# Kernel tuning notes

Hardware: AMD Instinct MI355X
Metric: run time of the kernel (lower is better)

The kernel has to match this reference:

```python
import jax, jax.numpy as jnp
import numpy as np

N, D, NUM_CLASSES = 4096, 512, 128
MARGIN = 0.3


def setup_inputs() -> dict:
    key = jax.random.key(0)
    k1, k2 = jax.random.split(key)
    embeddings = jax.random.normal(k1, (N, D), dtype=jnp.float32)
    labels = jax.random.randint(k2, (N,), 0, NUM_CLASSES, dtype=jnp.int64)
    return {"embeddings": embeddings, "labels": labels}


def _batch_hard_triplet(embeddings, labels, margin):
    # L2-normalize rows (torch F.normalize: x / max(||x||, eps))
    norm = jnp.linalg.norm(embeddings, axis=1, keepdims=True)
    e = embeddings / jnp.maximum(norm, 1e-12)
    n = e.shape[0]
    # Pairwise Euclidean distance via Gram matrix; ||a-b||^2 = 2 - 2 a.b for unit vectors
    gram = e @ e.T                                   # [N, N]
    sq = jnp.clip(2.0 - 2.0 * gram, 0.0, None)
    # safe sqrt: zero (and exactly-equal) pairs get distance 0 with zero gradient
    nz = sq > 0
    dist = jnp.where(nz, jnp.sqrt(jnp.where(nz, sq, 1.0)), 0.0)  # [N, N]

    same = labels[:, None] == labels[None, :]        # [N, N] bool
    eye = jnp.eye(n, dtype=bool)
    pos_mask = same & ~eye                           # positives excluding self
    neg_mask = ~same

    # hardest positive (row max over positives), hardest negative (row min over negatives)
    dist_ap = jnp.max(jnp.where(pos_mask, dist, -jnp.inf), axis=1)  # [N]
    dist_an = jnp.min(jnp.where(neg_mask, dist, jnp.inf), axis=1)   # [N]

    valid = jnp.any(pos_mask, axis=1) & jnp.any(neg_mask, axis=1)   # rows kept by torch loop
    per_row = jax.nn.relu(dist_ap - dist_an + margin)
    num_valid = jnp.sum(valid)
    loss_sum = jnp.sum(jnp.where(valid, per_row, 0.0))
    return jnp.where(num_valid > 0, loss_sum / jnp.maximum(num_valid, 1), 0.0)


def reference(embeddings, labels):
    return _batch_hard_triplet(embeddings, labels, MARGIN)
```

## Files before the change

### kernel.cpp

```cpp
#include <hip/hip_runtime.h>
#include <hip/hip_bf16.h>
#include <stdint.h>


#define NROW 4096
#define DIM  512
#define MARGIN 0.3f
#define BT 128
#define BK 32
#define NTILE (NROW / BT)
#define NPAIR (NTILE * (NTILE + 1) / 2)
#define POS_INIT 0xFFFFFFFFu
#define NEG_INIT 0u

typedef __attribute__((ext_vector_type(8))) __bf16 bf16x8;
typedef __attribute__((ext_vector_type(4))) float  f32x4;

__device__ __forceinline__ unsigned enc(float f) {
    unsigned u = __float_as_uint(f);
    return (u & 0x80000000u) ? ~u : (u | 0x80000000u);
}
__device__ __forceinline__ float dec(unsigned e) {
    return (e & 0x80000000u) ? __uint_as_float(e & 0x7fffffffu)
                             : __uint_as_float(~e);
}

__device__ __forceinline__ unsigned short f2bf(float f) {
    __hip_bfloat16 h = __float2bfloat16(f);
    return *reinterpret_cast<unsigned short*>(&h);
}

__device__ __forceinline__ void async_copy16(const void* g, void* l) {
    __builtin_amdgcn_global_load_lds(
        (const __attribute__((address_space(1))) unsigned int*)g,
        (__attribute__((address_space(3))) unsigned int*)l,
        16, 0, 0);
}

__global__ void tl_norm(const float* __restrict__ E,
                        __hip_bfloat16* __restrict__ Ebf,
                        unsigned* __restrict__ posArr,
                        unsigned* __restrict__ negArr) {
    if (blockIdx.x < 16) {
        int t = blockIdx.x * 256 + threadIdx.x;
        posArr[t] = POS_INIT;
        negArr[t] = NEG_INIT;
    }
    int wave = threadIdx.x >> 6;
    int lane = threadIdx.x & 63;
    int row  = blockIdx.x * 4 + wave;

    const float4* src = (const float4*)(E + (size_t)row * DIM);
    float4 v0 = src[lane];
    float4 v1 = src[lane + 64];
    float ss = v0.x*v0.x + v0.y*v0.y + v0.z*v0.z + v0.w*v0.w
             + v1.x*v1.x + v1.y*v1.y + v1.z*v1.z + v1.w*v1.w;
    #pragma unroll
    for (int m = 32; m >= 1; m >>= 1) ss += __shfl_xor(ss, m);
    float inv = 1.0f / fmaxf(sqrtf(ss), 1e-12f);

    ushort4 o0, o1;
    o0.x = f2bf(v0.x * inv); o0.y = f2bf(v0.y * inv);
    o0.z = f2bf(v0.z * inv); o0.w = f2bf(v0.w * inv);
    o1.x = f2bf(v1.x * inv); o1.y = f2bf(v1.y * inv);
    o1.z = f2bf(v1.z * inv); o1.w = f2bf(v1.w * inv);
    ushort4* dst = (ushort4*)(Ebf + (size_t)row * DIM);
    dst[lane]      = o0;
    dst[lane + 64] = o1;
}

__global__ void tl_gram(const __hip_bfloat16* __restrict__ Ebf,
                        const int* __restrict__ labels,
                        unsigned* __restrict__ posArr,
                        unsigned* __restrict__ negArr) {
    __shared__ __align__(16) __hip_bfloat16 At[BT * BK];
    __shared__ __align__(16) __hip_bfloat16 Bt[BT * BK];
    __shared__ int rowLab[BT];
    __shared__ int colLab[BT];

    int t = blockIdx.x, bi = 0, rowlen = NTILE;
    while (t >= rowlen) { t -= rowlen; rowlen--; bi++; }
    const int bj = bi + t;

    const int tid  = threadIdx.x;
    const int wave = tid >> 6;
    const int lane = tid & 63;
    const int quad = lane >> 4;
    const int l16  = lane & 15;
    const int wr   = wave >> 1;
    const int wc   = wave & 1;
    const int tileI = bi * BT;
    const int tileJ = bj * BT;
    const bool diag = (bi == bj);

    if (tid < BT) rowLab[tid] = labels[tileI + tid];
    else          colLab[tid - BT] = labels[tileJ + (tid - BT)];

    const int sRow = wave * 32 + (lane >> 2);
    const int sK   = (lane & 3) * 8;
    const __hip_bfloat16* gA = Ebf + (size_t)(tileI + sRow) * DIM + sK;
    const __hip_bfloat16* gB = Ebf + (size_t)(tileJ + sRow) * DIM + sK;
    __hip_bfloat16* lA0 = &At[(wave * 2 + 0) * 512];
    __hip_bfloat16* lA1 = &At[(wave * 2 + 1) * 512];
    __hip_bfloat16* lB0 = &Bt[(wave * 2 + 0) * 512];
    __hip_bfloat16* lB1 = &Bt[(wave * 2 + 1) * 512];

    f32x4 acc[4][4] = {};

    for (int k0 = 0; k0 < DIM; k0 += BK) {
        async_copy16(gA + k0,            lA0);
        async_copy16(gA + k0 + 16 * DIM, lA1);
        async_copy16(gB + k0,            lB0);
        async_copy16(gB + k0 + 16 * DIM, lB1);
        __syncthreads();

        bf16x8 a[4], b[4];
        #pragma unroll
        for (int mi = 0; mi < 4; mi++)
            a[mi] = *(const bf16x8*)&At[(wr * 64 + mi * 16 + l16) * BK + quad * 8];
        #pragma unroll
        for (int ni = 0; ni < 4; ni++)
            b[ni] = *(const bf16x8*)&Bt[(wc * 64 + ni * 16 + l16) * BK + quad * 8];

        #pragma unroll
        for (int mi = 0; mi < 4; mi++)
            #pragma unroll
            for (int ni = 0; ni < 4; ni++)
                acc[mi][ni] = __builtin_amdgcn_mfma_f32_16x16x32_bf16(
                    a[mi], b[ni], acc[mi][ni], 0, 0, 0);

        __syncthreads();
    }

    int rl[16], cl[4], clocv[4];
    #pragma unroll
    for (int mi = 0; mi < 4; mi++)
        #pragma unroll
        for (int reg = 0; reg < 4; reg++)
            rl[mi * 4 + reg] = rowLab[wr * 64 + mi * 16 + quad * 4 + reg];
    #pragma unroll
    for (int ni = 0; ni < 4; ni++) {
        clocv[ni] = wc * 64 + ni * 16 + l16;
        cl[ni] = colLab[clocv[ni]];
    }

    #pragma unroll
    for (int mi = 0; mi < 4; mi++) {
        #pragma unroll
        for (int reg = 0; reg < 4; reg++) {
            const int rloc = wr * 64 + mi * 16 + quad * 4 + reg;
            const int lr   = rl[mi * 4 + reg];
            const int gi   = tileI + rloc;
            float pmin =  INFINITY;
            float nmax = -INFINITY;
            #pragma unroll
            for (int ni = 0; ni < 4; ni++) {
                const int gj  = tileJ + clocv[ni];
                const float g = acc[mi][ni][reg];
                const bool same = (lr == cl[ni]);
                if (same && gi != gj) pmin = fminf(pmin, g);
                if (!same)            nmax = fmaxf(nmax, g);
            }
            #pragma unroll
            for (int m = 1; m < 16; m <<= 1) {
                pmin = fminf(pmin, __shfl_xor(pmin, m));
                nmax = fmaxf(nmax, __shfl_xor(nmax, m));
            }
            if (l16 == 0) {
                if (pmin <  INFINITY) atomicMin(&posArr[gi], enc(pmin));
                if (nmax > -INFINITY) atomicMax(&negArr[gi], enc(nmax));
            }
        }
    }

    if (!diag) {
        #pragma unroll
        for (int ni = 0; ni < 4; ni++) {
            const int lc = cl[ni];
            const int gj = tileJ + clocv[ni];
            float pmin =  INFINITY;
            float nmax = -INFINITY;
            #pragma unroll
            for (int mi = 0; mi < 4; mi++) {
                #pragma unroll
                for (int reg = 0; reg < 4; reg++) {
                    const float g = acc[mi][ni][reg];
                    const bool same = (rl[mi * 4 + reg] == lc);
                    if (same) pmin = fminf(pmin, g);
                    else      nmax = fmaxf(nmax, g);
                }
            }
            pmin = fminf(pmin, __shfl_xor(pmin, 16));
            pmin = fminf(pmin, __shfl_xor(pmin, 32));
            nmax = fmaxf(nmax, __shfl_xor(nmax, 16));
            nmax = fmaxf(nmax, __shfl_xor(nmax, 32));
            if (quad == 0) {
                if (pmin <  INFINITY) atomicMin(&posArr[gj], enc(pmin));
                if (nmax > -INFINITY) atomicMax(&negArr[gj], enc(nmax));
            }
        }
    }
}

__global__ void tl_final(const unsigned* __restrict__ posArr,
                         const unsigned* __restrict__ negArr,
                         float* __restrict__ out) {
    const int tid = threadIdx.x;
    float sum = 0.0f;
    int   count = 0;
    for (int i = tid; i < NROW; i += 256) {
        const unsigned pe = posArr[i];
        const unsigned ne = negArr[i];
        const bool valid = (pe != POS_INIT) && (ne != NEG_INIT);
        const float dap = sqrtf(fmaxf(2.0f - 2.0f * dec(pe), 0.0f));
        const float dan = sqrtf(fmaxf(2.0f - 2.0f * dec(ne), 0.0f));
        const float per = fmaxf(dap - dan + MARGIN, 0.0f);
        if (valid) { sum += per; count += 1; }
    }
    #pragma unroll
    for (int m = 32; m >= 1; m >>= 1) {
        sum   += __shfl_xor(sum, m);
        count += __shfl_xor(count, m);
    }
    __shared__ float ssum[4];
    __shared__ int   scnt[4];
    const int wave = tid >> 6, lane = tid & 63;
    if (lane == 0) { ssum[wave] = sum; scnt[wave] = count; }
    __syncthreads();
    if (tid == 0) {
        float s = ssum[0] + ssum[1] + ssum[2] + ssum[3];
        int   c = scnt[0] + scnt[1] + scnt[2] + scnt[3];
        out[0] = (c > 0) ? (s / (float)c) : 0.0f;
    }
}

extern "C" void kernel_launch(void* const* d_in, const int* in_sizes, int n_in,
                              void* d_out, int out_size, void* d_ws, size_t ws_size,
                              hipStream_t stream) {
    const float* E      = (const float*)d_in[0];
    const int*   labels = (const int*)d_in[1];
    float*       out    = (float*)d_out;

    char* ws = (char*)d_ws;
    __hip_bfloat16* Ebf   = (__hip_bfloat16*)ws;
    unsigned* posArr      = (unsigned*)(ws + (size_t)NROW * DIM * 2);
    unsigned* negArr      = posArr + NROW;

    tl_norm<<<NROW / 4, 256, 0, stream>>>(E, Ebf, posArr, negArr);
    tl_gram<<<NPAIR, 256, 0, stream>>>(Ebf, labels, posArr, negArr);
    tl_final<<<1, 256, 0, stream>>>(posArr, negArr, out);
}
```

Baseline: 93.43 us.

## Double-buffer LDS tiles in gram kernel and fuse final reduction via last-block counter

Double-buffers the A/B LDS tiles so the async global-to-LDS copies for the next K slice are issued before the MFMAs of the current slice. This leaves one barrier per iteration instead of two. It also folds the final loss reduction into the gram kernel: an atomic completion counter elects the last block, which reads the pos/neg arrays and writes the output, removing a separate launch. The cost is twice the LDS for tiles, which may lower occupancy, plus a threadfence and an atomic per block.

Measured after the change: 116.6 us. +24.8%, slower.

```diff
diff --git a/kernel.cpp b/kernel.cpp
--- a/kernel.cpp
+++ b/kernel.cpp
@@ -8,6 +8,7 @@
 #define MARGIN 0.3f
 #define BT 128
 #define BK 32
+#define KITERS (DIM / BK)
 #define NTILE (NROW / BT)
 #define NPAIR (NTILE * (NTILE + 1) / 2)
 #define POS_INIT 0xFFFFFFFFu
@@ -40,11 +41,13 @@
 __global__ void tl_norm(const float* __restrict__ E,
                         __hip_bfloat16* __restrict__ Ebf,
                         unsigned* __restrict__ posArr,
-                        unsigned* __restrict__ negArr) {
+                        unsigned* __restrict__ negArr,
+                        unsigned* __restrict__ doneCnt) {
     if (blockIdx.x < 16) {
         int t = blockIdx.x * 256 + threadIdx.x;
         posArr[t] = POS_INIT;
         negArr[t] = NEG_INIT;
+        if (t == 0) *doneCnt = 0;
     }
     int wave = threadIdx.x >> 6;
     int lane = threadIdx.x & 63;
@@ -72,11 +75,16 @@
 __global__ void tl_gram(const __hip_bfloat16* __restrict__ Ebf,
                         const int* __restrict__ labels,
                         unsigned* __restrict__ posArr,
-                        unsigned* __restrict__ negArr) {
-    __shared__ __align__(16) __hip_bfloat16 At[BT * BK];
-    __shared__ __align__(16) __hip_bfloat16 Bt[BT * BK];
+                        unsigned* __restrict__ negArr,
+                        unsigned* __restrict__ doneCnt,
+                        float* __restrict__ out) {
+    __shared__ __align__(16) __hip_bfloat16 At[2][BT * BK];
+    __shared__ __align__(16) __hip_bfloat16 Bt[2][BT * BK];
     __shared__ int rowLab[BT];
     __shared__ int colLab[BT];
+    __shared__ int lastFlag;
+    __shared__ float ssum[4];
+    __shared__ int   scnt[4];
 
     int t = blockIdx.x, bi = 0, rowlen = NTILE;
     while (t >= rowlen) { t -= rowlen; rowlen--; bi++; }
@@ -100,27 +108,36 @@
     const int sK   = (lane & 3) * 8;
     const __hip_bfloat16* gA = Ebf + (size_t)(tileI + sRow) * DIM + sK;
     const __hip_bfloat16* gB = Ebf + (size_t)(tileJ + sRow) * DIM + sK;
-    __hip_bfloat16* lA0 = &At[(wave * 2 + 0) * 512];
-    __hip_bfloat16* lA1 = &At[(wave * 2 + 1) * 512];
-    __hip_bfloat16* lB0 = &Bt[(wave * 2 + 0) * 512];
-    __hip_bfloat16* lB1 = &Bt[(wave * 2 + 1) * 512];
+    const int ldsOff0 = (wave * 2 + 0) * 512;
+    const int ldsOff1 = (wave * 2 + 1) * 512;
 
     f32x4 acc[4][4] = {};
 
-    for (int k0 = 0; k0 < DIM; k0 += BK) {
-        async_copy16(gA + k0,            lA0);
-        async_copy16(gA + k0 + 16 * DIM, lA1);
-        async_copy16(gB + k0,            lB0);
-        async_copy16(gB + k0 + 16 * DIM, lB1);
+    async_copy16(gA,            &At[0][ldsOff0]);
+    async_copy16(gA + 16 * DIM, &At[0][ldsOff1]);
+    async_copy16(gB,            &Bt[0][ldsOff0]);
+    async_copy16(gB + 16 * DIM, &Bt[0][ldsOff1]);
+
+    for (int it = 0; it < KITERS; it++) {
         __syncthreads();
 
+        if (it + 1 < KITERS) {
+            const int k1 = (it + 1) * BK;
+            const int nb = (it + 1) & 1;
+            async_copy16(gA + k1,            &At[nb][ldsOff0]);
+            async_copy16(gA + k1 + 16 * DIM, &At[nb][ldsOff1]);
+            async_copy16(gB + k1,            &Bt[nb][ldsOff0]);
+            async_copy16(gB + k1 + 16 * DIM, &Bt[nb][ldsOff1]);
+        }
+
+        const int cb = it & 1;
         bf16x8 a[4], b[4];
         #pragma unroll
         for (int mi = 0; mi < 4; mi++)
-            a[mi] = *(const bf16x8*)&At[(wr * 64 + mi * 16 + l16) * BK + quad * 8];
+            a[mi] = *(const bf16x8*)&At[cb][(wr * 64 + mi * 16 + l16) * BK + quad * 8];
         #pragma unroll
         for (int ni = 0; ni < 4; ni++)
-            b[ni] = *(const bf16x8*)&Bt[(wc * 64 + ni * 16 + l16) * BK + quad * 8];
+            b[ni] = *(const bf16x8*)&Bt[cb][(wc * 64 + ni * 16 + l16) * BK + quad * 8];
 
         #pragma unroll
         for (int mi = 0; mi < 4; mi++)
@@ -128,8 +145,6 @@
             for (int ni = 0; ni < 4; ni++)
                 acc[mi][ni] = __builtin_amdgcn_mfma_f32_16x16x32_bf16(
                     a[mi], b[ni], acc[mi][ni], 0, 0, 0);
-
-        __syncthreads();
     }
 
     int rl[16], cl[4], clocv[4];
@@ -200,37 +215,38 @@
             }
         }
     }
-}
-
-__global__ void tl_final(const unsigned* __restrict__ posArr,
-                         const unsigned* __restrict__ negArr,
-                         float* __restrict__ out) {
-    const int tid = threadIdx.x;
-    float sum = 0.0f;
-    int   count = 0;
-    for (int i = tid; i < NROW; i += 256) {
-        const unsigned pe = posArr[i];
-        const unsigned ne = negArr[i];
-        const bool valid = (pe != POS_INIT) && (ne != NEG_INIT);
-        const float dap = sqrtf(fmaxf(2.0f - 2.0f * dec(pe), 0.0f));
-        const float dan = sqrtf(fmaxf(2.0f - 2.0f * dec(ne), 0.0f));
-        const float per = fmaxf(dap - dan + MARGIN, 0.0f);
-        if (valid) { sum += per; count += 1; }
-    }
-    #pragma unroll
-    for (int m = 32; m >= 1; m >>= 1) {
-        sum   += __shfl_xor(sum, m);
-        count += __shfl_xor(count, m);
-    }
-    __shared__ float ssum[4];
-    __shared__ int   scnt[4];
-    const int wave = tid >> 6, lane = tid & 63;
-    if (lane == 0) { ssum[wave] = sum; scnt[wave] = count; }
+
+    __threadfence();
+    if (tid == 0) {
+        unsigned prev = atomicAdd(doneCnt, 1u);
+        lastFlag = (prev == NPAIR - 1) ? 1 : 0;
+    }
     __syncthreads();
-    if (tid == 0) {
-        float s = ssum[0] + ssum[1] + ssum[2] + ssum[3];
-        int   c = scnt[0] + scnt[1] + scnt[2] + scnt[3];
-        out[0] = (c > 0) ? (s / (float)c) : 0.0f;
+    if (lastFlag) {
+        __threadfence();
+        float sum = 0.0f;
+        int   count = 0;
+        for (int i = tid; i < NROW; i += 256) {
+            const unsigned pe = atomicOr(&posArr[i], 0u);
+            const unsigned ne = atomicOr(&negArr[i], 0u);
+            const bool valid = (pe != POS_INIT) && (ne != NEG_INIT);
+            const float dap = sqrtf(fmaxf(2.0f - 2.0f * dec(pe), 0.0f));
+            const float dan = sqrtf(fmaxf(2.0f - 2.0f * dec(ne), 0.0f));
+            const float per = fmaxf(dap - dan + MARGIN, 0.0f);
+            if (valid) { sum += per; count += 1; }
+        }
+        #pragma unroll
+        for (int m = 32; m >= 1; m >>= 1) {
+            sum   += __shfl_xor(sum, m);
+            count += __shfl_xor(count, m);
+        }
+        if (lane == 0) { ssum[wave] = sum; scnt[wave] = count; }
+        __syncthreads();
+        if (tid == 0) {
+            float s = ssum[0] + ssum[1] + ssum[2] + ssum[3];
+            int   c = scnt[0] + scnt[1] + scnt[2] + scnt[3];
+            out[0] = (c > 0) ? (s / (float)c) : 0.0f;
+        }
     }
 }
 
@@ -245,8 +261,8 @@
     __hip_bfloat16* Ebf   = (__hip_bfloat16*)ws;
     unsigned* posArr      = (unsigned*)(ws + (size_t)NROW * DIM * 2);
     unsigned* negArr      = posArr + NROW;
-
-    tl_norm<<<NROW / 4, 256, 0, stream>>>(E, Ebf, posArr, negArr);
-    tl_gram<<<NPAIR, 256, 0, stream>>>(Ebf, labels, posArr, negArr);
-    tl_final<<<1, 256, 0, stream>>>(posArr, negArr, out);
-}
+    unsigned* doneCnt     = negArr + NROW;
+
+    tl_norm<<<NROW / 4, 256, 0, stream>>>(E, Ebf, posArr, negArr, doneCnt);
+    tl_gram<<<NPAIR, 256, 0, stream>>>(Ebf, labels, posArr, negArr, doneCnt, out);
+}
```

## Load MFMA operands directly from global memory instead of staging through LDS

Applied to the files above, without the earlier changes.

The gram kernel no longer stages A/B tiles into shared memory with async global-to-LDS copies and barriers. Each lane now reads its bf16x8 fragments straight from global memory, and the fully unrolled K loop has no __syncthreads. This removes LDS traffic and barrier stalls, and launch bounds are added for two blocks per SIMD. The cost is that operand data shared between the waves of a block is no longer reused and must come from global memory or cache. The unrolled loop also adds register pressure and exposes global load latency.

New measurement: 118.7 us. +27.0%, slower.

```diff
diff --git a/kernel.cpp b/kernel.cpp
--- a/kernel.cpp
+++ b/kernel.cpp
@@ -7,7 +7,7 @@
 #define DIM  512
 #define MARGIN 0.3f
 #define BT 128
-#define BK 32
+#define KITERS 16
 #define NTILE (NROW / BT)
 #define NPAIR (NTILE * (NTILE + 1) / 2)
 #define POS_INIT 0xFFFFFFFFu
@@ -28,13 +28,6 @@
 __device__ __forceinline__ unsigned short f2bf(float f) {
     __hip_bfloat16 h = __float2bfloat16(f);
     return *reinterpret_cast<unsigned short*>(&h);
-}
-
-__device__ __forceinline__ void async_copy16(const void* g, void* l) {
-    __builtin_amdgcn_global_load_lds(
-        (const __attribute__((address_space(1))) unsigned int*)g,
-        (__attribute__((address_space(3))) unsigned int*)l,
-        16, 0, 0);
 }
 
 __global__ void tl_norm(const float* __restrict__ E,
@@ -69,12 +62,11 @@
     dst[lane + 64] = o1;
 }
 
-__global__ void tl_gram(const __hip_bfloat16* __restrict__ Ebf,
-                        const int* __restrict__ labels,
-                        unsigned* __restrict__ posArr,
-                        unsigned* __restrict__ negArr) {
-    __shared__ __align__(16) __hip_bfloat16 At[BT * BK];
-    __shared__ __align__(16) __hip_bfloat16 Bt[BT * BK];
+__global__ void __launch_bounds__(256, 2)
+tl_gram(const __hip_bfloat16* __restrict__ Ebf,
+        const int* __restrict__ labels,
+        unsigned* __restrict__ posArr,
+        unsigned* __restrict__ negArr) {
     __shared__ int rowLab[BT];
     __shared__ int colLab[BT];
 
@@ -95,32 +87,28 @@
 
     if (tid < BT) rowLab[tid] = labels[tileI + tid];
     else          colLab[tid - BT] = labels[tileJ + (tid - BT)];
-
-    const int sRow = wave * 32 + (lane >> 2);
-    const int sK   = (lane & 3) * 8;
-    const __hip_bfloat16* gA = Ebf + (size_t)(tileI + sRow) * DIM + sK;
-    const __hip_bfloat16* gB = Ebf + (size_t)(tileJ + sRow) * DIM + sK;
-    __hip_bfloat16* lA0 = &At[(wave * 2 + 0) * 512];
-    __hip_bfloat16* lA1 = &At[(wave * 2 + 1) * 512];
-    __hip_bfloat16* lB0 = &Bt[(wave * 2 + 0) * 512];
-    __hip_bfloat16* lB1 = &Bt[(wave * 2 + 1) * 512];
+    __syncthreads();
+
+    const __hip_bfloat16* aP[4];
+    const __hip_bfloat16* bP[4];
+    #pragma unroll
+    for (int mi = 0; mi < 4; mi++)
+        aP[mi] = Ebf + (size_t)(tileI + wr * 64 + mi * 16 + l16) * DIM + quad * 8;
+    #pragma unroll
+    for (int ni = 0; ni < 4; ni++)
+        bP[ni] = Ebf + (size_t)(tileJ + wc * 64 + ni * 16 + l16) * DIM + quad * 8;
 
     f32x4 acc[4][4] = {};
 
-    for (int k0 = 0; k0 < DIM; k0 += BK) {
-        async_copy16(gA + k0,            lA0);
-        async_copy16(gA + k0 + 16 * DIM, lA1);
-        async_copy16(gB + k0,            lB0);
-        async_copy16(gB + k0 + 16 * DIM, lB1);
-        __syncthreads();
-
+    #pragma unroll
+    for (int it = 0; it < KITERS; it++) {
         bf16x8 a[4], b[4];
         #pragma unroll
         for (int mi = 0; mi < 4; mi++)
-            a[mi] = *(const bf16x8*)&At[(wr * 64 + mi * 16 + l16) * BK + quad * 8];
+            a[mi] = *(const bf16x8*)(aP[mi] + it * 32);
         #pragma unroll
         for (int ni = 0; ni < 4; ni++)
-            b[ni] = *(const bf16x8*)&Bt[(wc * 64 + ni * 16 + l16) * BK + quad * 8];
+            b[ni] = *(const bf16x8*)(bP[ni] + it * 32);
 
         #pragma unroll
         for (int mi = 0; mi < 4; mi++)
@@ -128,8 +116,6 @@
             for (int ni = 0; ni < 4; ni++)
                 acc[mi][ni] = __builtin_amdgcn_mfma_f32_16x16x32_bf16(
                     a[mi], b[ni], acc[mi][ni], 0, 0, 0);
-
-        __syncthreads();
     }
 
     int rl[16], cl[4], clocv[4];
```
